# Performance work log

Measured on AMD Instinct MI355X. Metric: run time of the kernel, lower is better.

Reference implementation:

```python
import jax, jax.numpy as jnp
import numpy as np

TOPK_RATIO = 0.2
ALIGN_WEIGHT = 1.0
REG_WEIGHT = 0.1
EPS_LN = 1e-6
EPS_COS = 1e-8


def setup_inputs() -> dict:
    key = jax.random.key(0)
    k1, k2, k3, k4, k5 = jax.random.split(key, 5)
    B, C, H, W = 8, 256, 200, 200
    return {
        "bev_map": jax.random.normal(k1, (B, C, H, W), dtype=jnp.float32),
        "prior_warp": jax.random.normal(k2, (B, C, H, W), dtype=jnp.float32),
        "dx_m": jax.random.normal(k3, (B,), dtype=jnp.float32),
        "dy_m": jax.random.normal(k4, (B,), dtype=jnp.float32),
        "dtheta": jax.random.normal(k5, (B,), dtype=jnp.float32),
    }


def _channel_layer_norm(x):
    # per-pixel mean/std over channel dim; torch std is unbiased (ddof=1)
    mu = jnp.mean(x, axis=1, keepdims=True)
    sigma = jnp.std(x, axis=1, keepdims=True, ddof=1) + EPS_LN
    return (x - mu) / sigma


def reference(bev_map, prior_warp, dx_m, dy_m, dtheta):
    B, C, H, W = bev_map.shape
    bev_norm = _channel_layer_norm(bev_map)      # [B,C,H,W]
    prior_norm = _channel_layer_norm(prior_warp)  # [B,C,H,W]

    # squared-sum score per pixel, flattened over spatial dims
    score = jnp.sum(bev_map * bev_map, axis=1).reshape(B, H * W)  # [B,HW]
    k = max(1, int(TOPK_RATIO * H * W))
    _, idx = jax.lax.top_k(score, k)             # [B,k]

    idx_bc = jnp.broadcast_to(idx[:, None, :], (B, C, k))
    bev_topk = jnp.take_along_axis(bev_norm.reshape(B, C, H * W), idx_bc, axis=2)
    prior_topk = jnp.take_along_axis(prior_norm.reshape(B, C, H * W), idx_bc, axis=2)

    # cosine similarity over channel dim (torch eps semantics: clamp each norm)
    num = jnp.sum(bev_topk * prior_topk, axis=1)                       # [B,k]
    na = jnp.sqrt(jnp.sum(bev_topk * bev_topk, axis=1))
    nb = jnp.sqrt(jnp.sum(prior_topk * prior_topk, axis=1))
    sim = num / (jnp.maximum(na, EPS_COS) * jnp.maximum(nb, EPS_COS))
    align_loss = jnp.mean(1.0 - sim)

    reg_loss = jnp.mean(dx_m * dx_m + dy_m * dy_m) + jnp.mean(dtheta * dtheta)
    return ALIGN_WEIGHT * align_loss + REG_WEIGHT * reg_loss
```

## Files before the change

kernel.cpp:

```cpp
#include <hip/hip_runtime.h>
#include <math.h>

#define BATCH 8
#define CCH 256
#define HW 40000
#define HW4 (HW / 4)
#define KSEL 8000
#define EPS_LN 1e-6f
#define EPS_COS 1e-8f
#define SLICES 40
#define SLICE_LEN (HW / SLICES)

#define OFF_SCORE   0
#define OFF_CONTRIB 320000
#define OFF_HIST1   640000
#define OFF_HIST2   1164288
#define OFF_PREFIX  1688576
#define OFF_REM1    1688584
#define OFF_TKEY    1688592
#define OFF_REM2    1688600
#define OFF_TIE     1688608
#define OFF_BSUMS   1688616

typedef float v4f __attribute__((ext_vector_type(4)));

__device__ __forceinline__ unsigned int mono_key(float x) {
  unsigned int u = __float_as_uint(x);
  return (u & 0x80000000u) ? ~u : (u | 0x80000000u);
}

__global__ __launch_bounds__(256) void zero_kernel(unsigned int* __restrict__ ws) {
  const int n4 = (2 * BATCH * 65536) / 4;
  uint4* p = (uint4*)(ws + OFF_HIST1);
  uint4 z = {0u, 0u, 0u, 0u};
  for (int i = blockIdx.x * blockDim.x + threadIdx.x; i < n4; i += gridDim.x * blockDim.x)
    p[i] = z;
  if (blockIdx.x == 0 && threadIdx.x < BATCH) ws[OFF_BSUMS + threadIdx.x] = 0u;
}

__global__ __launch_bounds__(256) void pixel_stats_kernel(
    const float* __restrict__ A, const float* __restrict__ B,
    float* __restrict__ score, float* __restrict__ contrib,
    unsigned int* __restrict__ ws) {
  int tid = blockIdx.x * blockDim.x + threadIdx.x;
  if (tid >= BATCH * HW4) return;
  int b = tid / HW4;
  int p4 = tid - b * HW4;
  const v4f* a  = (const v4f*)(A + (size_t)b * CCH * HW) + p4;
  const v4f* bb = (const v4f*)(B + (size_t)b * CCH * HW) + p4;

  float sa[4] = {0, 0, 0, 0}, ssa[4] = {0, 0, 0, 0};
  float sb[4] = {0, 0, 0, 0}, ssb[4] = {0, 0, 0, 0}, dab[4] = {0, 0, 0, 0};
#pragma unroll 8
  for (int c = 0; c < CCH; ++c) {
    v4f x = __builtin_nontemporal_load(a + (size_t)c * HW4);
    v4f y = __builtin_nontemporal_load(bb + (size_t)c * HW4);
#pragma unroll
    for (int j = 0; j < 4; ++j) {
      float xs = x[j], ys = y[j];
      sa[j] += xs;
      ssa[j] = fmaf(xs, xs, ssa[j]);
      sb[j] += ys;
      ssb[j] = fmaf(ys, ys, ssb[j]);
      dab[j] = fmaf(xs, ys, dab[j]);
    }
  }

  float scv[4], cov[4];
  const float invC = 1.0f / (float)CCH;
#pragma unroll
  for (int j = 0; j < 4; ++j) {
    scv[j] = ssa[j];
    float mua = sa[j] * invC, mub = sb[j] * invC;
    float cssa = fmaxf(ssa[j] - (float)CCH * mua * mua, 0.f);
    float cssb = fmaxf(ssb[j] - (float)CCH * mub * mub, 0.f);
    float cdot = dab[j] - (float)CCH * mua * mub;
    float siga = sqrtf(cssa / (float)(CCH - 1)) + EPS_LN;
    float sigb = sqrtf(cssb / (float)(CCH - 1)) + EPS_LN;
    float num = cdot / (siga * sigb);
    float na = sqrtf(cssa) / siga;
    float nb = sqrtf(cssb) / sigb;
    cov[j] = 1.0f - num / (fmaxf(na, EPS_COS) * fmaxf(nb, EPS_COS));
  }
  int out = b * HW + p4 * 4;
  *(v4f*)(score + out)   = (v4f){scv[0], scv[1], scv[2], scv[3]};
  *(v4f*)(contrib + out) = (v4f){cov[0], cov[1], cov[2], cov[3]};

  unsigned int* h1 = ws + OFF_HIST1 + (b << 16);
#pragma unroll
  for (int j = 0; j < 4; ++j)
    atomicAdd(&h1[mono_key(scv[j]) >> 16], 1u);
}

__global__ __launch_bounds__(256) void hist2_kernel(
    const float* __restrict__ score, unsigned int* __restrict__ ws) {
  int b = blockIdx.x / SLICES;
  int sl = blockIdx.x - b * SLICES;
  const float* s = score + b * HW;
  unsigned int pref = ws[OFF_PREFIX + b];
  unsigned int* h = ws + OFF_HIST2 + (b << 16);
  int base = sl * SLICE_LEN;
  for (int i = base + threadIdx.x; i < base + SLICE_LEN; i += 256) {
    unsigned int key = mono_key(s[i]);
    if ((key >> 16) == pref) atomicAdd(&h[key & 0xFFFFu], 1u);
  }
}

__global__ __launch_bounds__(1024) void select_kernel(unsigned int* __restrict__ ws,
                                                      int phase) {
  int b = blockIdx.x;
  const unsigned int* h = ws + (phase ? OFF_HIST2 : OFF_HIST1) + (b << 16);
  unsigned int K = phase ? ws[OFF_REM1 + b] : (unsigned int)KSEL;

  __shared__ unsigned int chunk[1024];
  __shared__ unsigned int suf[1024];
  __shared__ unsigned int s_chunk_idx, s_cum_above;
  __shared__ unsigned int bins[64];

  int t = threadIdx.x;
  unsigned int sum = 0;
#pragma unroll 8
  for (int i = 0; i < 64; ++i) sum += h[t * 64 + i];
  chunk[t] = sum;
  suf[t] = sum;
  __syncthreads();
  for (int off = 1; off < 1024; off <<= 1) {
    unsigned int v = (t + off < 1024) ? suf[t + off] : 0u;
    __syncthreads();
    suf[t] += v;
    __syncthreads();
  }
  unsigned int above = (t == 1023) ? 0u : suf[t + 1];
  if (suf[t] >= K && above < K) { s_chunk_idx = (unsigned int)t; s_cum_above = above; }
  __syncthreads();
  if (t < 64) bins[t] = h[s_chunk_idx * 64 + t];
  __syncthreads();
  if (t == 0) {
    unsigned int cum = s_cum_above;
    int d = 63;
    for (; d >= 0; --d) {
      if (cum + bins[d] >= K) break;
      cum += bins[d];
    }
    unsigned int binidx = s_chunk_idx * 64 + (unsigned int)d;
    if (phase == 0) {
      ws[OFF_PREFIX + b] = binidx;
      ws[OFF_REM1 + b] = K - cum;
    } else {
      ws[OFF_TKEY + b] = (ws[OFF_PREFIX + b] << 16) | binidx;
      ws[OFF_REM2 + b] = K - cum;
      ws[OFF_TIE + b] = 0u;
    }
  }
}

__global__ __launch_bounds__(256) void sum_kernel(
    const float* __restrict__ score, const float* __restrict__ contrib,
    unsigned int* __restrict__ ws) {
  int b = blockIdx.x / SLICES;
  int sl = blockIdx.x - b * SLICES;
  const float* s = score + b * HW;
  const float* ct = contrib + b * HW;
  unsigned int T = ws[OFF_TKEY + b];
  unsigned int rem2 = ws[OFF_REM2 + b];

  float partial = 0.f;
  int base = sl * SLICE_LEN;
  for (int i = base + threadIdx.x; i < base + SLICE_LEN; i += 256) {
    unsigned int key = mono_key(s[i]);
    if (key > T) {
      partial += ct[i];
    } else if (key == T) {
      unsigned int old = atomicAdd(&ws[OFF_TIE + b], 1u);
      if (old < rem2) partial += ct[i];
    }
  }

  __shared__ float red[256];
  red[threadIdx.x] = partial;
  __syncthreads();
  for (int off = 128; off > 0; off >>= 1) {
    if (threadIdx.x < (unsigned)off) red[threadIdx.x] += red[threadIdx.x + off];
    __syncthreads();
  }
  if (threadIdx.x == 0) atomicAdd((float*)(ws + OFF_BSUMS) + b, red[0]);
}

__global__ void finalize_kernel(const unsigned int* __restrict__ ws,
                                const float* __restrict__ dx,
                                const float* __restrict__ dy,
                                const float* __restrict__ dth,
                                float* __restrict__ out) {
  if (threadIdx.x == 0 && blockIdx.x == 0) {
    const float* bsums = (const float*)(ws + OFF_BSUMS);
    float s = 0.f;
    for (int b = 0; b < BATCH; ++b) s += bsums[b];
    float align = s / (float)(BATCH * KSEL);
    float r1 = 0.f, r2 = 0.f;
    for (int b = 0; b < BATCH; ++b) {
      r1 += dx[b] * dx[b] + dy[b] * dy[b];
      r2 += dth[b] * dth[b];
    }
    out[0] = align + 0.1f * (r1 / (float)BATCH + r2 / (float)BATCH);
  }
}

extern "C" void kernel_launch(void* const* d_in, const int* in_sizes, int n_in,
                              void* d_out, int out_size, void* d_ws, size_t ws_size,
                              hipStream_t stream) {
  const float* bev   = (const float*)d_in[0];
  const float* prior = (const float*)d_in[1];
  const float* dx    = (const float*)d_in[2];
  const float* dy    = (const float*)d_in[3];
  const float* dth   = (const float*)d_in[4];
  float* out = (float*)d_out;

  unsigned int* ws = (unsigned int*)d_ws;
  float* score   = (float*)ws + OFF_SCORE;
  float* contrib = (float*)ws + OFF_CONTRIB;

  zero_kernel<<<256, 256, 0, stream>>>(ws);
  pixel_stats_kernel<<<(BATCH * HW4 + 255) / 256, 256, 0, stream>>>(bev, prior, score, contrib, ws);
  select_kernel<<<BATCH, 1024, 0, stream>>>(ws, 0);
  hist2_kernel<<<BATCH * SLICES, 256, 0, stream>>>(score, ws);
  select_kernel<<<BATCH, 1024, 0, stream>>>(ws, 1);
  sum_kernel<<<BATCH * SLICES, 256, 0, stream>>>(score, contrib, ws);
  finalize_kernel<<<1, 64, 0, stream>>>(ws, dx, dy, dth, out);
}
```

Baseline: 710.5 us.

## Fuse radix-select passes into one per-batch kernel and double-buffer channel loads

Replaces the second global histogram, two select launches and the sum kernel with a single per-batch 1024-thread kernel. It refines the top-k threshold with two 8-bit shared-memory histogram passes over precomputed monotone keys, then sums the selected contributions. The stats kernel now stores keys instead of raw scores and software-pipelines the channel loads with double-buffered register arrays of 8 channels each. Launch count and global atomics drop, but the tail now runs on only 8 blocks, each rescanning 40000 keys three times. The larger register footprint of the pipelined loop may also cut occupancy.

```diff
diff --git a/kernel.cpp b/kernel.cpp
--- a/kernel.cpp
+++ b/kernel.cpp
@@ -8,21 +8,14 @@
 #define KSEL 8000
 #define EPS_LN 1e-6f
 #define EPS_COS 1e-8f
-#define SLICES 40
-#define SLICE_LEN (HW / SLICES)
-
-#define OFF_SCORE   0
+
+#define OFF_KEYS    0
 #define OFF_CONTRIB 320000
 #define OFF_HIST1   640000
-#define OFF_HIST2   1164288
-#define OFF_PREFIX  1688576
-#define OFF_REM1    1688584
-#define OFF_TKEY    1688592
-#define OFF_REM2    1688600
-#define OFF_TIE     1688608
-#define OFF_BSUMS   1688616
+#define OFF_BSUMS   1164288
 
 typedef float v4f __attribute__((ext_vector_type(4)));
+#define NT(p) __builtin_nontemporal_load(p)
 
 __device__ __forceinline__ unsigned int mono_key(float x) {
   unsigned int u = __float_as_uint(x);
@@ -30,7 +23,7 @@
 }
 
 __global__ __launch_bounds__(256) void zero_kernel(unsigned int* __restrict__ ws) {
-  const int n4 = (2 * BATCH * 65536) / 4;
+  const int n4 = (BATCH * 65536) / 4;
   uint4* p = (uint4*)(ws + OFF_HIST1);
   uint4 z = {0u, 0u, 0u, 0u};
   for (int i = blockIdx.x * blockDim.x + threadIdx.x; i < n4; i += gridDim.x * blockDim.x)
@@ -38,9 +31,9 @@
   if (blockIdx.x == 0 && threadIdx.x < BATCH) ws[OFF_BSUMS + threadIdx.x] = 0u;
 }
 
-__global__ __launch_bounds__(256) void pixel_stats_kernel(
+__global__ __launch_bounds__(256, 1) void pixel_stats_kernel(
     const float* __restrict__ A, const float* __restrict__ B,
-    float* __restrict__ score, float* __restrict__ contrib,
+    unsigned int* __restrict__ keys, float* __restrict__ contrib,
     unsigned int* __restrict__ ws) {
   int tid = blockIdx.x * blockDim.x + threadIdx.x;
   if (tid >= BATCH * HW4) return;
@@ -51,26 +44,57 @@
 
   float sa[4] = {0, 0, 0, 0}, ssa[4] = {0, 0, 0, 0};
   float sb[4] = {0, 0, 0, 0}, ssb[4] = {0, 0, 0, 0}, dab[4] = {0, 0, 0, 0};
-#pragma unroll 8
-  for (int c = 0; c < CCH; ++c) {
-    v4f x = __builtin_nontemporal_load(a + (size_t)c * HW4);
-    v4f y = __builtin_nontemporal_load(bb + (size_t)c * HW4);
-#pragma unroll
-    for (int j = 0; j < 4; ++j) {
-      float xs = x[j], ys = y[j];
-      sa[j] += xs;
-      ssa[j] = fmaf(xs, xs, ssa[j]);
-      sb[j] += ys;
-      ssb[j] = fmaf(ys, ys, ssb[j]);
-      dab[j] = fmaf(xs, ys, dab[j]);
-    }
-  }
-
-  float scv[4], cov[4];
+
+  v4f xA[8], yA[8], xB[8], yB[8];
+#pragma unroll
+  for (int k = 0; k < 8; ++k) {
+    xA[k] = NT(a + (size_t)k * HW4);
+    yA[k] = NT(bb + (size_t)k * HW4);
+  }
+
+#pragma unroll 1
+  for (int it = 0; it < 16; ++it) {
+    const size_t cb = (size_t)it * 16;
+#pragma unroll
+    for (int k = 0; k < 8; ++k) {
+      xB[k] = NT(a + (cb + 8 + (size_t)k) * HW4);
+      yB[k] = NT(bb + (cb + 8 + (size_t)k) * HW4);
+    }
+#pragma unroll
+    for (int k = 0; k < 8; ++k) {
+#pragma unroll
+      for (int j = 0; j < 4; ++j) {
+        float xs = xA[k][j], ys = yA[k][j];
+        sa[j] += xs;  ssa[j] = fmaf(xs, xs, ssa[j]);
+        sb[j] += ys;  ssb[j] = fmaf(ys, ys, ssb[j]);
+        dab[j] = fmaf(xs, ys, dab[j]);
+      }
+    }
+    if (it < 15) {
+#pragma unroll
+      for (int k = 0; k < 8; ++k) {
+        xA[k] = NT(a + (cb + 16 + (size_t)k) * HW4);
+        yA[k] = NT(bb + (cb + 16 + (size_t)k) * HW4);
+      }
+    }
+#pragma unroll
+    for (int k = 0; k < 8; ++k) {
+#pragma unroll
+      for (int j = 0; j < 4; ++j) {
+        float xs = xB[k][j], ys = yB[k][j];
+        sa[j] += xs;  ssa[j] = fmaf(xs, xs, ssa[j]);
+        sb[j] += ys;  ssb[j] = fmaf(ys, ys, ssb[j]);
+        dab[j] = fmaf(xs, ys, dab[j]);
+      }
+    }
+  }
+
+  unsigned int kv[4];
+  float cov[4];
   const float invC = 1.0f / (float)CCH;
 #pragma unroll
   for (int j = 0; j < 4; ++j) {
-    scv[j] = ssa[j];
+    kv[j] = mono_key(ssa[j]);
     float mua = sa[j] * invC, mub = sb[j] * invC;
     float cssa = fmaxf(ssa[j] - (float)CCH * mua * mua, 0.f);
     float cssb = fmaxf(ssb[j] - (float)CCH * mub * mub, 0.f);
@@ -83,107 +107,123 @@
     cov[j] = 1.0f - num / (fmaxf(na, EPS_COS) * fmaxf(nb, EPS_COS));
   }
   int out = b * HW + p4 * 4;
-  *(v4f*)(score + out)   = (v4f){scv[0], scv[1], scv[2], scv[3]};
+  *(uint4*)(keys + out)  = make_uint4(kv[0], kv[1], kv[2], kv[3]);
   *(v4f*)(contrib + out) = (v4f){cov[0], cov[1], cov[2], cov[3]};
 
   unsigned int* h1 = ws + OFF_HIST1 + (b << 16);
 #pragma unroll
   for (int j = 0; j < 4; ++j)
-    atomicAdd(&h1[mono_key(scv[j]) >> 16], 1u);
-}
-
-__global__ __launch_bounds__(256) void hist2_kernel(
-    const float* __restrict__ score, unsigned int* __restrict__ ws) {
-  int b = blockIdx.x / SLICES;
-  int sl = blockIdx.x - b * SLICES;
-  const float* s = score + b * HW;
-  unsigned int pref = ws[OFF_PREFIX + b];
-  unsigned int* h = ws + OFF_HIST2 + (b << 16);
-  int base = sl * SLICE_LEN;
-  for (int i = base + threadIdx.x; i < base + SLICE_LEN; i += 256) {
-    unsigned int key = mono_key(s[i]);
-    if ((key >> 16) == pref) atomicAdd(&h[key & 0xFFFFu], 1u);
-  }
-}
-
-__global__ __launch_bounds__(1024) void select_kernel(unsigned int* __restrict__ ws,
-                                                      int phase) {
+    atomicAdd(&h1[kv[j] >> 16], 1u);
+}
+
+__global__ __launch_bounds__(1024) void select_sum_kernel(
+    const unsigned int* __restrict__ keys, const float* __restrict__ contrib,
+    unsigned int* __restrict__ ws) {
   int b = blockIdx.x;
-  const unsigned int* h = ws + (phase ? OFF_HIST2 : OFF_HIST1) + (b << 16);
-  unsigned int K = phase ? ws[OFF_REM1 + b] : (unsigned int)KSEL;
-
-  __shared__ unsigned int chunk[1024];
+  int t = threadIdx.x;
+  const unsigned int* kb = keys + b * HW;
+  const float* cbp = contrib + b * HW;
+
   __shared__ unsigned int suf[1024];
-  __shared__ unsigned int s_chunk_idx, s_cum_above;
   __shared__ unsigned int bins[64];
-
-  int t = threadIdx.x;
-  unsigned int sum = 0;
+  __shared__ unsigned int hbin[256];
+  __shared__ unsigned int s_idx, s_above;
+  __shared__ unsigned int s_tie;
+
+  unsigned int prefix, K;
+
+  {
+    const unsigned int* h = ws + OFF_HIST1 + (b << 16);
+    unsigned int sum = 0;
 #pragma unroll 8
-  for (int i = 0; i < 64; ++i) sum += h[t * 64 + i];
-  chunk[t] = sum;
-  suf[t] = sum;
+    for (int i = 0; i < 64; ++i) sum += h[t * 64 + i];
+    suf[t] = sum;
+    __syncthreads();
+    for (int off = 1; off < 1024; off <<= 1) {
+      unsigned int v = (t + off < 1024) ? suf[t + off] : 0u;
+      __syncthreads();
+      suf[t] += v;
+      __syncthreads();
+    }
+    unsigned int above = (t == 1023) ? 0u : suf[t + 1];
+    if (suf[t] >= (unsigned)KSEL && above < (unsigned)KSEL) { s_idx = (unsigned)t; s_above = above; }
+    __syncthreads();
+    if (t < 64) bins[t] = h[s_idx * 64 + t];
+    __syncthreads();
+    if (t == 0) {
+      unsigned int cum = s_above;
+      int d = 63;
+      for (; d >= 0; --d) {
+        if (cum + bins[d] >= (unsigned)KSEL) break;
+        cum += bins[d];
+      }
+      s_idx = s_idx * 64 + (unsigned)d;
+      s_above = cum;
+    }
+    __syncthreads();
+    prefix = s_idx;
+    K = (unsigned)KSEL - s_above;
+    __syncthreads();
+  }
+
+#pragma unroll 1
+  for (int pass = 0; pass < 2; ++pass) {
+    if (t < 256) hbin[t] = 0u;
+    __syncthreads();
+    if (pass == 0) {
+      for (int i = t; i < HW; i += 1024) {
+        unsigned int key = kb[i];
+        if ((key >> 16) == prefix) atomicAdd(&hbin[(key >> 8) & 0xFFu], 1u);
+      }
+    } else {
+      for (int i = t; i < HW; i += 1024) {
+        unsigned int key = kb[i];
+        if ((key >> 8) == prefix) atomicAdd(&hbin[key & 0xFFu], 1u);
+      }
+    }
+    __syncthreads();
+    if (t < 256) suf[t] = hbin[t];
+    __syncthreads();
+    for (int off = 1; off < 256; off <<= 1) {
+      unsigned int v = (t < 256 && t + off < 256) ? suf[t + off] : 0u;
+      __syncthreads();
+      if (t < 256) suf[t] += v;
+      __syncthreads();
+    }
+    if (t < 256) {
+      unsigned int above = (t == 255) ? 0u : suf[t + 1];
+      if (suf[t] >= K && above < K) { s_idx = (unsigned)t; s_above = above; }
+    }
+    __syncthreads();
+    prefix = (prefix << 8) | s_idx;
+    K = K - s_above;
+    __syncthreads();
+  }
+
+  const unsigned int T = prefix;
+  const unsigned int rem2 = K;
+  if (t == 0) s_tie = 0u;
   __syncthreads();
-  for (int off = 1; off < 1024; off <<= 1) {
-    unsigned int v = (t + off < 1024) ? suf[t + off] : 0u;
-    __syncthreads();
-    suf[t] += v;
-    __syncthreads();
-  }
-  unsigned int above = (t == 1023) ? 0u : suf[t + 1];
-  if (suf[t] >= K && above < K) { s_chunk_idx = (unsigned int)t; s_cum_above = above; }
+
+  float partial = 0.f;
+  for (int i = t; i < HW; i += 1024) {
+    unsigned int key = kb[i];
+    if (key > T) {
+      partial += cbp[i];
+    } else if (key == T) {
+      unsigned int old = atomicAdd(&s_tie, 1u);
+      if (old < rem2) partial += cbp[i];
+    }
+  }
   __syncthreads();
-  if (t < 64) bins[t] = h[s_chunk_idx * 64 + t];
+  float* redf = (float*)suf;
+  redf[t] = partial;
   __syncthreads();
-  if (t == 0) {
-    unsigned int cum = s_cum_above;
-    int d = 63;
-    for (; d >= 0; --d) {
-      if (cum + bins[d] >= K) break;
-      cum += bins[d];
-    }
-    unsigned int binidx = s_chunk_idx * 64 + (unsigned int)d;
-    if (phase == 0) {
-      ws[OFF_PREFIX + b] = binidx;
-      ws[OFF_REM1 + b] = K - cum;
-    } else {
-      ws[OFF_TKEY + b] = (ws[OFF_PREFIX + b] << 16) | binidx;
-      ws[OFF_REM2 + b] = K - cum;
-      ws[OFF_TIE + b] = 0u;
-    }
-  }
-}
-
-__global__ __launch_bounds__(256) void sum_kernel(
-    const float* __restrict__ score, const float* __restrict__ contrib,
-    unsigned int* __restrict__ ws) {
-  int b = blockIdx.x / SLICES;
-  int sl = blockIdx.x - b * SLICES;
-  const float* s = score + b * HW;
-  const float* ct = contrib + b * HW;
-  unsigned int T = ws[OFF_TKEY + b];
-  unsigned int rem2 = ws[OFF_REM2 + b];
-
-  float partial = 0.f;
-  int base = sl * SLICE_LEN;
-  for (int i = base + threadIdx.x; i < base + SLICE_LEN; i += 256) {
-    unsigned int key = mono_key(s[i]);
-    if (key > T) {
-      partial += ct[i];
-    } else if (key == T) {
-      unsigned int old = atomicAdd(&ws[OFF_TIE + b], 1u);
-      if (old < rem2) partial += ct[i];
-    }
-  }
-
-  __shared__ float red[256];
-  red[threadIdx.x] = partial;
-  __syncthreads();
-  for (int off = 128; off > 0; off >>= 1) {
-    if (threadIdx.x < (unsigned)off) red[threadIdx.x] += red[threadIdx.x + off];
-    __syncthreads();
-  }
-  if (threadIdx.x == 0) atomicAdd((float*)(ws + OFF_BSUMS) + b, red[0]);
+  for (int off = 512; off > 0; off >>= 1) {
+    if (t < off) redf[t] += redf[t + off];
+    __syncthreads();
+  }
+  if (t == 0) ((float*)(ws + OFF_BSUMS))[b] = redf[0];
 }
 
 __global__ void finalize_kernel(const unsigned int* __restrict__ ws,
@@ -216,14 +256,11 @@
   float* out = (float*)d_out;
 
   unsigned int* ws = (unsigned int*)d_ws;
-  float* score   = (float*)ws + OFF_SCORE;
-  float* contrib = (float*)ws + OFF_CONTRIB;
+  unsigned int* keys = ws + OFF_KEYS;
+  float* contrib     = (float*)ws + OFF_CONTRIB;
 
   zero_kernel<<<256, 256, 0, stream>>>(ws);
-  pixel_stats_kernel<<<(BATCH * HW4 + 255) / 256, 256, 0, stream>>>(bev, prior, score, contrib, ws);
-  select_kernel<<<BATCH, 1024, 0, stream>>>(ws, 0);
-  hist2_kernel<<<BATCH * SLICES, 256, 0, stream>>>(score, ws);
-  select_kernel<<<BATCH, 1024, 0, stream>>>(ws, 1);
-  sum_kernel<<<BATCH * SLICES, 256, 0, stream>>>(score, contrib, ws);
+  pixel_stats_kernel<<<(BATCH * HW4 + 255) / 256, 256, 0, stream>>>(bev, prior, keys, contrib, ws);
+  select_sum_kernel<<<BATCH, 1024, 0, stream>>>(keys, contrib, ws);
   finalize_kernel<<<1, 64, 0, stream>>>(ws, dx, dy, dth, out);
 }
```

Measured after the change: 733.9 us. +3.3%, slower.
